# Kernel optimization log

Hardware: AMD Instinct MI355X
Metric: run time of the kernel (lower is better)

## Reference

```python
import jax, jax.numpy as jnp
import numpy as np

B, C, T, H, NCLS = 512, 22, 1000, 64, 4


def setup_inputs() -> dict:
    key = jax.random.key(0)
    ks = jax.random.split(key, 8)
    s_ih = 1.0 / np.sqrt(H)
    x = jax.random.normal(ks[0], (B, C, T), dtype=jnp.float32)
    # PyTorch LSTM params: gate order [i, f, g, o], each of size H
    W_ih = jax.random.uniform(ks[1], (4 * H, C), minval=-s_ih, maxval=s_ih, dtype=jnp.float32)
    W_hh = jax.random.uniform(ks[2], (4 * H, H), minval=-s_ih, maxval=s_ih, dtype=jnp.float32)
    b_ih = jax.random.uniform(ks[3], (4 * H,), minval=-s_ih, maxval=s_ih, dtype=jnp.float32)
    b_hh = jax.random.uniform(ks[4], (4 * H,), minval=-s_ih, maxval=s_ih, dtype=jnp.float32)
    s_fc = 1.0 / np.sqrt(H * T)
    W_fc = jax.random.uniform(ks[5], (NCLS, H * T), minval=-s_fc, maxval=s_fc, dtype=jnp.float32)
    b_fc = jax.random.uniform(ks[6], (NCLS,), minval=-s_fc, maxval=s_fc, dtype=jnp.float32)
    return {"x": x, "W_ih": W_ih, "W_hh": W_hh, "b_ih": b_ih, "b_hh": b_hh,
            "W_fc": W_fc, "b_fc": b_fc}


def _lstm(xs, W_ih, W_hh, b_ih, b_hh):
    # xs: [B, T, C] -> outputs [B, T, H]
    b = xs.shape[0]
    # precompute input projections for all timesteps: [T, B, 4H]
    x_proj = jnp.einsum('btc,gc->tbg', xs, W_ih) + (b_ih + b_hh)
    h0 = jnp.zeros((b, W_hh.shape[1]), xs.dtype)
    c0 = jnp.zeros_like(h0)

    def step(carry, xp):
        h, c = carry
        gates = xp + h @ W_hh.T  # [B, 4H]
        i, f, g, o = jnp.split(gates, 4, axis=-1)
        i = jax.nn.sigmoid(i)
        f = jax.nn.sigmoid(f)
        g = jnp.tanh(g)
        o = jax.nn.sigmoid(o)
        c = f * c + i * g
        h = o * jnp.tanh(c)
        return (h, c), h

    _, hs = jax.lax.scan(step, (h0, c0), x_proj)  # hs: [T, B, H]
    return jnp.transpose(hs, (1, 0, 2))  # [B, T, H]


def reference(x, W_ih, W_hh, b_ih, b_hh, W_fc, b_fc):
    xs = jnp.transpose(x, (0, 2, 1))  # [B, T, C]  (permute(0,2,1))
    hs = _lstm(xs, W_ih, W_hh, b_ih, b_hh)  # [B, T, H]
    flat = hs.reshape(hs.shape[0], -1)  # [B, T*H], time-major per row
    logits = flat @ W_fc.T + b_fc  # [B, 4]
    return jax.nn.softmax(logits, axis=1)
```

## Files before the change

kernel.cpp:

```cpp
#include <hip/hip_runtime.h>

#define BB   512
#define CC   22
#define TT   1000
#define HH   64
#define NCLS 4
#define FCW  (TT * HH)
#define TB   100

typedef _Float16 f16;
typedef __attribute__((ext_vector_type(2))) _Float16 h2;

__device__ __forceinline__ float sigm(float x) {
    float e = __expf(-x);
    return __builtin_amdgcn_rcpf(1.0f + e);
}
__device__ __forceinline__ float tanh_(float x) {
    float e = __expf(-2.0f * fabsf(x));
    float r = (1.0f - e) * __builtin_amdgcn_rcpf(1.0f + e);
    return copysignf(r, x);
}
__device__ __forceinline__ h2 u2h(unsigned u) {
    union { unsigned u; h2 h; } c; c.u = u; return c.h;
}
__device__ __forceinline__ unsigned h2u(h2 h) {
    union { unsigned u; h2 h; } c; c.h = h; return c.u;
}

__global__ __launch_bounds__(256) void xproj(
    const float* __restrict__ x,
    const float* __restrict__ W_ih,
    const float* __restrict__ b_ih,
    const float* __restrict__ b_hh,
    f16* __restrict__ xp)
{
    __shared__ __align__(16) float xt[CC][TB];

    const int tid = threadIdx.x;
    const int t0  = blockIdx.x * TB;
    const int b   = blockIdx.y;
    const int hid = tid >> 2;
    const int g   = tid & 3;
    const int row = g * HH + hid;

    for (int s = tid; s < CC * TB; s += 256) {
        const int c = s / TB, t = s - c * TB;
        xt[c][t] = x[((size_t)b * CC + c) * TT + t0 + t];
    }
    float wr[CC];
    #pragma unroll
    for (int c = 0; c < CC; ++c) wr[c] = W_ih[row * CC + c];
    const float bias = b_ih[row] + b_hh[row];
    __syncthreads();

    f16* op = xp + ((size_t)b * TT + t0) * 256 + tid;
    for (int t = 0; t < TB; t += 4) {
        float a0 = bias, a1 = bias, a2 = bias, a3 = bias;
        #pragma unroll
        for (int c = 0; c < CC; ++c) {
            const float4 xv = *(const float4*)&xt[c][t];
            a0 += wr[c] * xv.x; a1 += wr[c] * xv.y;
            a2 += wr[c] * xv.z; a3 += wr[c] * xv.w;
        }
        op[0]   = (f16)a0;
        op[256] = (f16)a1;
        op[512] = (f16)a2;
        op[768] = (f16)a3;
        op += 1024;
    }
}

__global__ __attribute__((amdgpu_waves_per_eu(1, 1)))
__launch_bounds__(64) void lstm_rec(
    const uint2* __restrict__ xp,
    const float* __restrict__ W_hh,
    const float* __restrict__ W_fc,
    const float* __restrict__ b_fc,
    float* __restrict__ out)
{
    __shared__ __align__(16) f16 hbuf[HH];

    const int lane = threadIdx.x;
    const int r    = blockIdx.x;

    unsigned whh[4][32];
    #pragma unroll
    for (int g = 0; g < 4; ++g) {
        const float* wr = W_hh + (g * HH + lane) * HH;
        #pragma unroll
        for (int k = 0; k < 32; ++k)
            whh[g][k] = h2u(h2{(f16)wr[2 * k], (f16)wr[2 * k + 1]});
    }
    #pragma unroll
    for (int g = 0; g < 4; ++g)
        #pragma unroll
        for (int k = 0; k < 32; ++k) asm volatile("" : "+v"(whh[g][k]));

    hbuf[lane] = (f16)0.0f;
    float c = 0.0f;
    float fc0 = 0.f, fc1 = 0.f, fc2 = 0.f, fc3 = 0.f;
    const uint2* px = xp + (size_t)r * TT * HH + lane;
    const float* p0 = W_fc + 0 * FCW + lane;
    const float* p1 = W_fc + 1 * FCW + lane;
    const float* p2 = W_fc + 2 * FCW + lane;
    const float* p3 = W_fc + 3 * FCW + lane;

    for (int t = 0; t < TT; ++t) {
        const uint2 xv = px[(size_t)t * HH];
        const float w0 = *p0, w1 = *p1, w2 = *p2, w3 = *p3;
        p0 += HH; p1 += HH; p2 += HH; p3 += HH;

        union { uint4 q[8]; h2 h[32]; } H;
        const uint4* hr = (const uint4*)hbuf;
        #pragma unroll
        for (int i = 0; i < 8; ++i) H.q[i] = hr[i];

        float a0 = 0.f, a1 = 0.f, a2 = 0.f, a3 = 0.f;
        #pragma unroll
        for (int k = 0; k < 32; ++k) {
            a0 = __builtin_amdgcn_fdot2(H.h[k], u2h(whh[0][k]), a0, false);
            a1 = __builtin_amdgcn_fdot2(H.h[k], u2h(whh[1][k]), a1, false);
            a2 = __builtin_amdgcn_fdot2(H.h[k], u2h(whh[2][k]), a2, false);
            a3 = __builtin_amdgcn_fdot2(H.h[k], u2h(whh[3][k]), a3, false);
        }
        const h2 pif = u2h(xv.x), pgo = u2h(xv.y);
        a0 += (float)pif[0]; a1 += (float)pif[1];
        a2 += (float)pgo[0]; a3 += (float)pgo[1];

        const float iv = sigm(a0), fv = sigm(a1);
        const float gv = tanh_(a2), ov = sigm(a3);
        c = fv * c + iv * gv;
        const float h = ov * tanh_(c);

        fc0 += h * w0; fc1 += h * w1; fc2 += h * w2; fc3 += h * w3;

        hbuf[lane] = (f16)h;
    }

    #pragma unroll
    for (int off = 32; off; off >>= 1) {
        fc0 += __shfl_down(fc0, off);
        fc1 += __shfl_down(fc1, off);
        fc2 += __shfl_down(fc2, off);
        fc3 += __shfl_down(fc3, off);
    }
    if (lane == 0) {
        const float l0 = fc0 + b_fc[0], l1 = fc1 + b_fc[1];
        const float l2 = fc2 + b_fc[2], l3 = fc3 + b_fc[3];
        const float m  = fmaxf(fmaxf(l0, l1), fmaxf(l2, l3));
        const float e0 = __expf(l0 - m), e1 = __expf(l1 - m);
        const float e2 = __expf(l2 - m), e3 = __expf(l3 - m);
        const float is = __builtin_amdgcn_rcpf(e0 + e1 + e2 + e3);
        float4 o; o.x = e0 * is; o.y = e1 * is; o.z = e2 * is; o.w = e3 * is;
        *(float4*)(out + r * NCLS) = o;
    }
}

#define TC   250
#define NCHUNK (TT / TC)
#define XROW 12

__global__ __attribute__((amdgpu_waves_per_eu(1, 1)))
__launch_bounds__(64) void lstm_fb(
    const float* __restrict__ x, const float* __restrict__ W_ih,
    const float* __restrict__ W_hh, const float* __restrict__ b_ih,
    const float* __restrict__ b_hh, const float* __restrict__ W_fc,
    const float* __restrict__ b_fc, float* __restrict__ out)
{
    __shared__ __align__(16) h2  xs[TC][XROW];
    __shared__ __align__(16) f16 hbuf[HH];

    const int lane = threadIdx.x;
    const int r    = blockIdx.x;

    unsigned whh[4][32];
    unsigned wih[4][11];
    float bias[4];
    #pragma unroll
    for (int g = 0; g < 4; ++g) {
        const int row = g * HH + lane;
        const float* wr = W_hh + row * HH;
        #pragma unroll
        for (int k = 0; k < 32; ++k)
            whh[g][k] = h2u(h2{(f16)wr[2 * k], (f16)wr[2 * k + 1]});
        const float* wi = W_ih + row * CC;
        #pragma unroll
        for (int k = 0; k < 11; ++k)
            wih[g][k] = h2u(h2{(f16)wi[2 * k], (f16)wi[2 * k + 1]});
        bias[g] = b_ih[row] + b_hh[row];
    }
    #pragma unroll
    for (int g = 0; g < 4; ++g) {
        #pragma unroll
        for (int k = 0; k < 32; ++k) asm volatile("" : "+v"(whh[g][k]));
        #pragma unroll
        for (int k = 0; k < 11; ++k) asm volatile("" : "+v"(wih[g][k]));
        asm volatile("" : "+v"(bias[g]));
    }

    hbuf[lane] = (f16)0.0f;
    float c = 0.0f;
    float fc0 = 0.f, fc1 = 0.f, fc2 = 0.f, fc3 = 0.f;
    const float* p0 = W_fc + 0 * FCW + lane;
    const float* p1 = W_fc + 1 * FCW + lane;
    const float* p2 = W_fc + 2 * FCW + lane;
    const float* p3 = W_fc + 3 * FCW + lane;
    const float* xrow = x + (size_t)r * (CC * TT);

    for (int chunk = 0; chunk < NCHUNK; ++chunk) {
        for (int tb = 0; tb < TC; tb += 64) {
            const int t = tb + lane;
            if (t < TC) {
                const float* gx = xrow + chunk * TC + t;
                union { h2 h[XROW]; uint4 q[3]; } U;
                #pragma unroll
                for (int k = 0; k < 11; ++k)
                    U.h[k] = h2{(f16)gx[(2 * k) * TT], (f16)gx[(2 * k + 1) * TT]};
                U.h[11] = h2{(f16)0.0f, (f16)0.0f};
                uint4* dst = (uint4*)&xs[t][0];
                dst[0] = U.q[0]; dst[1] = U.q[1]; dst[2] = U.q[2];
            }
        }
        for (int tt = 0; tt < TC; ++tt) {
            union { uint4 q[8]; h2 h[32]; } H;
            const uint4* hr = (const uint4*)hbuf;
            #pragma unroll
            for (int i = 0; i < 8; ++i) H.q[i] = hr[i];
            union { uint4 q[3]; h2 h[XROW]; } X;
            const uint4* xr = (const uint4*)&xs[tt][0];
            X.q[0] = xr[0]; X.q[1] = xr[1]; X.q[2] = xr[2];
            float w0 = *p0, w1 = *p1, w2 = *p2, w3 = *p3;
            p0 += HH; p1 += HH; p2 += HH; p3 += HH;
            float a0 = bias[0], a1 = bias[1], a2 = bias[2], a3 = bias[3];
            #pragma unroll
            for (int k = 0; k < 11; ++k) {
                a0 = __builtin_amdgcn_fdot2(X.h[k], u2h(wih[0][k]), a0, false);
                a1 = __builtin_amdgcn_fdot2(X.h[k], u2h(wih[1][k]), a1, false);
                a2 = __builtin_amdgcn_fdot2(X.h[k], u2h(wih[2][k]), a2, false);
                a3 = __builtin_amdgcn_fdot2(X.h[k], u2h(wih[3][k]), a3, false);
            }
            #pragma unroll
            for (int k = 0; k < 32; ++k) {
                a0 = __builtin_amdgcn_fdot2(H.h[k], u2h(whh[0][k]), a0, false);
                a1 = __builtin_amdgcn_fdot2(H.h[k], u2h(whh[1][k]), a1, false);
                a2 = __builtin_amdgcn_fdot2(H.h[k], u2h(whh[2][k]), a2, false);
                a3 = __builtin_amdgcn_fdot2(H.h[k], u2h(whh[3][k]), a3, false);
            }
            const float iv = sigm(a0), fv = sigm(a1);
            const float gv = tanh_(a2), ov = sigm(a3);
            c = fv * c + iv * gv;
            const float h = ov * tanh_(c);
            fc0 += h * w0; fc1 += h * w1; fc2 += h * w2; fc3 += h * w3;
            hbuf[lane] = (f16)h;
        }
    }
    #pragma unroll
    for (int off = 32; off; off >>= 1) {
        fc0 += __shfl_down(fc0, off);
        fc1 += __shfl_down(fc1, off);
        fc2 += __shfl_down(fc2, off);
        fc3 += __shfl_down(fc3, off);
    }
    if (lane == 0) {
        const float l0 = fc0 + b_fc[0], l1 = fc1 + b_fc[1];
        const float l2 = fc2 + b_fc[2], l3 = fc3 + b_fc[3];
        const float m  = fmaxf(fmaxf(l0, l1), fmaxf(l2, l3));
        const float e0 = __expf(l0 - m), e1 = __expf(l1 - m);
        const float e2 = __expf(l2 - m), e3 = __expf(l3 - m);
        const float is = __builtin_amdgcn_rcpf(e0 + e1 + e2 + e3);
        float4 o; o.x = e0 * is; o.y = e1 * is; o.z = e2 * is; o.w = e3 * is;
        *(float4*)(out + r * NCLS) = o;
    }
}

extern "C" void kernel_launch(void* const* d_in, const int* in_sizes, int n_in,
                              void* d_out, int out_size, void* d_ws, size_t ws_size,
                              hipStream_t stream) {
    const float* x    = (const float*)d_in[0];
    const float* W_ih = (const float*)d_in[1];
    const float* W_hh = (const float*)d_in[2];
    const float* b_ih = (const float*)d_in[3];
    const float* b_hh = (const float*)d_in[4];
    const float* W_fc = (const float*)d_in[5];
    const float* b_fc = (const float*)d_in[6];
    float* out = (float*)d_out;

    const size_t need = (size_t)BB * TT * HH * 4 * sizeof(f16);
    if (d_ws != nullptr && ws_size >= need) {
        f16* xp = (f16*)d_ws;
        xproj<<<dim3(TT / TB, BB), 256, 0, stream>>>(x, W_ih, b_ih, b_hh, xp);
        lstm_rec<<<BB, 64, 0, stream>>>((const uint2*)xp, W_hh, W_fc, b_fc, out);
    } else {
        lstm_fb<<<BB, 64, 0, stream>>>(x, W_ih, W_hh, b_ih, b_hh, W_fc, b_fc, out);
    }
}
```

Before: 729.5 us.

## Prefetch projections two steps ahead, unroll recurrence by two, pack xproj stores

The recurrent loop is unrolled by two, and the input projections and FC weights for steps t+2 and t+3 are loaded ahead of time, so global memory latency is hidden behind the serial dot-product chain. The projection bias is now the initial value of the fdot2 accumulators instead of being added afterwards. The xproj kernel has each thread compute two gate rows and write them as one packed half2 word, halving the number of store instructions. The cost is higher register pressure in a kernel that already holds W_hh in registers, which could cause spills.

```diff
diff --git a/kernel.cpp b/kernel.cpp
--- a/kernel.cpp
+++ b/kernel.cpp
@@ -26,47 +26,61 @@
 __device__ __forceinline__ unsigned h2u(h2 h) {
     union { unsigned u; h2 h; } c; c.h = h; return c.u;
 }
+__device__ __forceinline__ unsigned pack2(float a, float b) {
+    union { unsigned u; h2 h; } c;
+    c.h = h2{(f16)a, (f16)b};
+    return c.u;
+}
 
 __global__ __launch_bounds__(256) void xproj(
     const float* __restrict__ x,
     const float* __restrict__ W_ih,
     const float* __restrict__ b_ih,
     const float* __restrict__ b_hh,
-    f16* __restrict__ xp)
+    unsigned* __restrict__ xp)
 {
     __shared__ __align__(16) float xt[CC][TB];
 
     const int tid = threadIdx.x;
     const int t0  = blockIdx.x * TB;
     const int b   = blockIdx.y;
-    const int hid = tid >> 2;
-    const int g   = tid & 3;
-    const int row = g * HH + hid;
+    const int th  = tid >> 7;
+    const int p   = tid & 127;
+    const int hid = p >> 1;
+    const int gp  = p & 1;
+    const int ra  = (2 * gp) * HH + hid;
+    const int rb  = (2 * gp + 1) * HH + hid;
 
     for (int s = tid; s < CC * TB; s += 256) {
         const int c = s / TB, t = s - c * TB;
         xt[c][t] = x[((size_t)b * CC + c) * TT + t0 + t];
     }
-    float wr[CC];
-    #pragma unroll
-    for (int c = 0; c < CC; ++c) wr[c] = W_ih[row * CC + c];
-    const float bias = b_ih[row] + b_hh[row];
+    float wa[CC], wb[CC];
+    #pragma unroll
+    for (int c = 0; c < CC; ++c) {
+        wa[c] = W_ih[ra * CC + c];
+        wb[c] = W_ih[rb * CC + c];
+    }
+    const float ba = b_ih[ra] + b_hh[ra];
+    const float bb = b_ih[rb] + b_hh[rb];
     __syncthreads();
 
-    f16* op = xp + ((size_t)b * TT + t0) * 256 + tid;
-    for (int t = 0; t < TB; t += 4) {
-        float a0 = bias, a1 = bias, a2 = bias, a3 = bias;
+    unsigned* op = xp + ((size_t)b * TT + t0) * 128 + p;
+    for (int tb = th * 4; tb < TB; tb += 8) {
+        float a0 = ba, a1 = ba, a2 = ba, a3 = ba;
+        float c0 = bb, c1 = bb, c2 = bb, c3 = bb;
         #pragma unroll
         for (int c = 0; c < CC; ++c) {
-            const float4 xv = *(const float4*)&xt[c][t];
-            a0 += wr[c] * xv.x; a1 += wr[c] * xv.y;
-            a2 += wr[c] * xv.z; a3 += wr[c] * xv.w;
-        }
-        op[0]   = (f16)a0;
-        op[256] = (f16)a1;
-        op[512] = (f16)a2;
-        op[768] = (f16)a3;
-        op += 1024;
+            const float4 xv = *(const float4*)&xt[c][tb];
+            a0 += wa[c] * xv.x; a1 += wa[c] * xv.y;
+            a2 += wa[c] * xv.z; a3 += wa[c] * xv.w;
+            c0 += wb[c] * xv.x; c1 += wb[c] * xv.y;
+            c2 += wb[c] * xv.z; c3 += wb[c] * xv.w;
+        }
+        op[(size_t)(tb + 0) * 128] = pack2(a0, c0);
+        op[(size_t)(tb + 1) * 128] = pack2(a1, c1);
+        op[(size_t)(tb + 2) * 128] = pack2(a2, c2);
+        op[(size_t)(tb + 3) * 128] = pack2(a3, c3);
     }
 }
 
@@ -100,41 +114,74 @@
     float c = 0.0f;
     float fc0 = 0.f, fc1 = 0.f, fc2 = 0.f, fc3 = 0.f;
     const uint2* px = xp + (size_t)r * TT * HH + lane;
-    const float* p0 = W_fc + 0 * FCW + lane;
-    const float* p1 = W_fc + 1 * FCW + lane;
-    const float* p2 = W_fc + 2 * FCW + lane;
-    const float* p3 = W_fc + 3 * FCW + lane;
-
-    for (int t = 0; t < TT; ++t) {
-        const uint2 xv = px[(size_t)t * HH];
-        const float w0 = *p0, w1 = *p1, w2 = *p2, w3 = *p3;
-        p0 += HH; p1 += HH; p2 += HH; p3 += HH;
-
-        union { uint4 q[8]; h2 h[32]; } H;
-        const uint4* hr = (const uint4*)hbuf;
-        #pragma unroll
-        for (int i = 0; i < 8; ++i) H.q[i] = hr[i];
-
-        float a0 = 0.f, a1 = 0.f, a2 = 0.f, a3 = 0.f;
-        #pragma unroll
-        for (int k = 0; k < 32; ++k) {
-            a0 = __builtin_amdgcn_fdot2(H.h[k], u2h(whh[0][k]), a0, false);
-            a1 = __builtin_amdgcn_fdot2(H.h[k], u2h(whh[1][k]), a1, false);
-            a2 = __builtin_amdgcn_fdot2(H.h[k], u2h(whh[2][k]), a2, false);
-            a3 = __builtin_amdgcn_fdot2(H.h[k], u2h(whh[3][k]), a3, false);
-        }
-        const h2 pif = u2h(xv.x), pgo = u2h(xv.y);
-        a0 += (float)pif[0]; a1 += (float)pif[1];
-        a2 += (float)pgo[0]; a3 += (float)pgo[1];
-
-        const float iv = sigm(a0), fv = sigm(a1);
-        const float gv = tanh_(a2), ov = sigm(a3);
-        c = fv * c + iv * gv;
-        const float h = ov * tanh_(c);
-
-        fc0 += h * w0; fc1 += h * w1; fc2 += h * w2; fc3 += h * w3;
-
-        hbuf[lane] = (f16)h;
+    const float* pf0 = W_fc + 0 * FCW + lane;
+    const float* pf1 = W_fc + 1 * FCW + lane;
+    const float* pf2 = W_fc + 2 * FCW + lane;
+    const float* pf3 = W_fc + 3 * FCW + lane;
+
+    uint2 xvA = px[0];
+    uint2 xvB = px[HH];
+    float wA0 = pf0[0],  wA1 = pf1[0],  wA2 = pf2[0],  wA3 = pf3[0];
+    float wB0 = pf0[HH], wB1 = pf1[HH], wB2 = pf2[HH], wB3 = pf3[HH];
+
+    for (int t = 0; t < TT; t += 2) {
+        const size_t o2 = (size_t)((t + 2 < TT) ? t + 2 : TT - 1) * HH;
+        const size_t o3 = (size_t)((t + 3 < TT) ? t + 3 : TT - 1) * HH;
+        const uint2 xv2 = px[o2];
+        const uint2 xv3 = px[o3];
+        const float w20 = pf0[o2], w21 = pf1[o2], w22 = pf2[o2], w23 = pf3[o2];
+        const float w30 = pf0[o3], w31 = pf1[o3], w32 = pf2[o3], w33 = pf3[o3];
+
+        {
+            union { uint4 q[8]; h2 h[32]; } H;
+            const uint4* hr = (const uint4*)hbuf;
+            #pragma unroll
+            for (int i = 0; i < 8; ++i) H.q[i] = hr[i];
+
+            const h2 pif = u2h(xvA.x), pgo = u2h(xvA.y);
+            float a0 = (float)pif[0], a1 = (float)pif[1];
+            float a2 = (float)pgo[0], a3 = (float)pgo[1];
+            #pragma unroll
+            for (int k = 0; k < 32; ++k) {
+                a0 = __builtin_amdgcn_fdot2(H.h[k], u2h(whh[0][k]), a0, false);
+                a1 = __builtin_amdgcn_fdot2(H.h[k], u2h(whh[1][k]), a1, false);
+                a2 = __builtin_amdgcn_fdot2(H.h[k], u2h(whh[2][k]), a2, false);
+                a3 = __builtin_amdgcn_fdot2(H.h[k], u2h(whh[3][k]), a3, false);
+            }
+            const float iv = sigm(a0), fv = sigm(a1);
+            const float gv = tanh_(a2), ov = sigm(a3);
+            c = fv * c + iv * gv;
+            const float h = ov * tanh_(c);
+            fc0 += h * wA0; fc1 += h * wA1; fc2 += h * wA2; fc3 += h * wA3;
+            hbuf[lane] = (f16)h;
+        }
+        {
+            union { uint4 q[8]; h2 h[32]; } H;
+            const uint4* hr = (const uint4*)hbuf;
+            #pragma unroll
+            for (int i = 0; i < 8; ++i) H.q[i] = hr[i];
+
+            const h2 pif = u2h(xvB.x), pgo = u2h(xvB.y);
+            float a0 = (float)pif[0], a1 = (float)pif[1];
+            float a2 = (float)pgo[0], a3 = (float)pgo[1];
+            #pragma unroll
+            for (int k = 0; k < 32; ++k) {
+                a0 = __builtin_amdgcn_fdot2(H.h[k], u2h(whh[0][k]), a0, false);
+                a1 = __builtin_amdgcn_fdot2(H.h[k], u2h(whh[1][k]), a1, false);
+                a2 = __builtin_amdgcn_fdot2(H.h[k], u2h(whh[2][k]), a2, false);
+                a3 = __builtin_amdgcn_fdot2(H.h[k], u2h(whh[3][k]), a3, false);
+            }
+            const float iv = sigm(a0), fv = sigm(a1);
+            const float gv = tanh_(a2), ov = sigm(a3);
+            c = fv * c + iv * gv;
+            const float h = ov * tanh_(c);
+            fc0 += h * wB0; fc1 += h * wB1; fc2 += h * wB2; fc3 += h * wB3;
+            hbuf[lane] = (f16)h;
+        }
+
+        xvA = xv2; xvB = xv3;
+        wA0 = w20; wA1 = w21; wA2 = w22; wA3 = w23;
+        wB0 = w30; wB1 = w31; wB2 = w32; wB3 = w33;
     }
 
     #pragma unroll
@@ -287,7 +334,7 @@
 
     const size_t need = (size_t)BB * TT * HH * 4 * sizeof(f16);
     if (d_ws != nullptr && ws_size >= need) {
-        f16* xp = (f16*)d_ws;
+        unsigned* xp = (unsigned*)d_ws;
         xproj<<<dim3(TT / TB, BB), 256, 0, stream>>>(x, W_ih, b_ih, b_hh, xp);
         lstm_rec<<<BB, 64, 0, stream>>>((const uint2*)xp, W_hh, W_fc, b_fc, out);
     } else {
```

Result: slower. 756.1 us (+3.6%).

## Defer FC reduction out of the recurrence, prefetch xproj, use fdot2 input projection

Applied to the files above, without the earlier changes.

The recurrent kernel no longer loads four W_fc values per step inside the serial time loop. It stores h for 250-step chunks in LDS and runs the FC dot product after each chunk. It also prefetches the input projection three steps ahead with a rotating register queue, and folds the projection into the accumulator init. The xproj kernel is reorganised to convert x and W_ih to fp16 pairs and use fdot2, writing packed uint2 per hidden unit, which adds fp16 rounding of the inputs and weights.

```diff
diff --git a/kernel.cpp b/kernel.cpp
--- a/kernel.cpp
+++ b/kernel.cpp
@@ -6,7 +6,8 @@
 #define HH   64
 #define NCLS 4
 #define FCW  (TT * HH)
-#define TB   100
+#define TBX  200
+#define TCF  250
 
 typedef _Float16 f16;
 typedef __attribute__((ext_vector_type(2))) _Float16 h2;
@@ -25,6 +26,11 @@
 }
 __device__ __forceinline__ unsigned h2u(h2 h) {
     union { unsigned u; h2 h; } c; c.h = h; return c.u;
+}
+__device__ __forceinline__ unsigned pack2(float a, float b) {
+    union { unsigned u; h2 h; } c;
+    c.h = h2{(f16)a, (f16)b};
+    return c.u;
 }
 
 __global__ __launch_bounds__(256) void xproj(
@@ -32,41 +38,53 @@
     const float* __restrict__ W_ih,
     const float* __restrict__ b_ih,
     const float* __restrict__ b_hh,
-    f16* __restrict__ xp)
+    uint2* __restrict__ xp)
 {
-    __shared__ __align__(16) float xt[CC][TB];
+    __shared__ __align__(16) h2 xt[TBX][12];
 
     const int tid = threadIdx.x;
-    const int t0  = blockIdx.x * TB;
+    const int t0  = blockIdx.x * TBX;
     const int b   = blockIdx.y;
-    const int hid = tid >> 2;
-    const int g   = tid & 3;
-    const int row = g * HH + hid;
-
-    for (int s = tid; s < CC * TB; s += 256) {
-        const int c = s / TB, t = s - c * TB;
-        xt[c][t] = x[((size_t)b * CC + c) * TT + t0 + t];
-    }
-    float wr[CC];
-    #pragma unroll
-    for (int c = 0; c < CC; ++c) wr[c] = W_ih[row * CC + c];
-    const float bias = b_ih[row] + b_hh[row];
+    const int hid = tid & 63;
+    const int tsub = tid >> 6;
+
+    if (tid < TBX) {
+        const float* gx = x + (size_t)b * (CC * TT) + t0 + tid;
+        union { h2 h[12]; uint4 q[3]; } U;
+        #pragma unroll
+        for (int k = 0; k < 11; ++k)
+            U.h[k] = h2{(f16)gx[(2 * k) * TT], (f16)gx[(2 * k + 1) * TT]};
+        U.h[11] = h2{(f16)0.0f, (f16)0.0f};
+        uint4* dst = (uint4*)&xt[tid][0];
+        dst[0] = U.q[0]; dst[1] = U.q[1]; dst[2] = U.q[2];
+    }
+
+    unsigned wih[4][11];
+    float bias[4];
+    #pragma unroll
+    for (int g = 0; g < 4; ++g) {
+        const float* wi = W_ih + (g * HH + hid) * CC;
+        #pragma unroll
+        for (int k = 0; k < 11; ++k)
+            wih[g][k] = h2u(h2{(f16)wi[2 * k], (f16)wi[2 * k + 1]});
+        bias[g] = b_ih[g * HH + hid] + b_hh[g * HH + hid];
+    }
     __syncthreads();
 
-    f16* op = xp + ((size_t)b * TT + t0) * 256 + tid;
-    for (int t = 0; t < TB; t += 4) {
-        float a0 = bias, a1 = bias, a2 = bias, a3 = bias;
-        #pragma unroll
-        for (int c = 0; c < CC; ++c) {
-            const float4 xv = *(const float4*)&xt[c][t];
-            a0 += wr[c] * xv.x; a1 += wr[c] * xv.y;
-            a2 += wr[c] * xv.z; a3 += wr[c] * xv.w;
-        }
-        op[0]   = (f16)a0;
-        op[256] = (f16)a1;
-        op[512] = (f16)a2;
-        op[768] = (f16)a3;
-        op += 1024;
+    uint2* op = xp + ((size_t)b * TT + t0) * 64 + hid;
+    for (int t = tsub; t < TBX; t += 4) {
+        union { uint4 q[3]; h2 h[12]; } X;
+        const uint4* xr = (const uint4*)&xt[t][0];
+        X.q[0] = xr[0]; X.q[1] = xr[1]; X.q[2] = xr[2];
+        float a0 = bias[0], a1 = bias[1], a2 = bias[2], a3 = bias[3];
+        #pragma unroll
+        for (int k = 0; k < 11; ++k) {
+            a0 = __builtin_amdgcn_fdot2(X.h[k], u2h(wih[0][k]), a0, false);
+            a1 = __builtin_amdgcn_fdot2(X.h[k], u2h(wih[1][k]), a1, false);
+            a2 = __builtin_amdgcn_fdot2(X.h[k], u2h(wih[2][k]), a2, false);
+            a3 = __builtin_amdgcn_fdot2(X.h[k], u2h(wih[3][k]), a3, false);
+        }
+        op[(size_t)t * 64] = uint2{pack2(a0, a1), pack2(a2, a3)};
     }
 }
 
@@ -78,7 +96,7 @@
     const float* __restrict__ b_fc,
     float* __restrict__ out)
 {
-    __shared__ __align__(16) f16 hbuf[HH];
+    __shared__ __align__(16) f16 hst[TCF][HH];
 
     const int lane = threadIdx.x;
     const int r    = blockIdx.x;
@@ -96,45 +114,62 @@
         #pragma unroll
         for (int k = 0; k < 32; ++k) asm volatile("" : "+v"(whh[g][k]));
 
-    hbuf[lane] = (f16)0.0f;
+    hst[TCF - 1][lane] = (f16)0.0f;
     float c = 0.0f;
     float fc0 = 0.f, fc1 = 0.f, fc2 = 0.f, fc3 = 0.f;
     const uint2* px = xp + (size_t)r * TT * HH + lane;
-    const float* p0 = W_fc + 0 * FCW + lane;
-    const float* p1 = W_fc + 1 * FCW + lane;
-    const float* p2 = W_fc + 2 * FCW + lane;
-    const float* p3 = W_fc + 3 * FCW + lane;
-
-    for (int t = 0; t < TT; ++t) {
-        const uint2 xv = px[(size_t)t * HH];
-        const float w0 = *p0, w1 = *p1, w2 = *p2, w3 = *p3;
-        p0 += HH; p1 += HH; p2 += HH; p3 += HH;
-
-        union { uint4 q[8]; h2 h[32]; } H;
-        const uint4* hr = (const uint4*)hbuf;
-        #pragma unroll
-        for (int i = 0; i < 8; ++i) H.q[i] = hr[i];
-
-        float a0 = 0.f, a1 = 0.f, a2 = 0.f, a3 = 0.f;
-        #pragma unroll
-        for (int k = 0; k < 32; ++k) {
-            a0 = __builtin_amdgcn_fdot2(H.h[k], u2h(whh[0][k]), a0, false);
-            a1 = __builtin_amdgcn_fdot2(H.h[k], u2h(whh[1][k]), a1, false);
-            a2 = __builtin_amdgcn_fdot2(H.h[k], u2h(whh[2][k]), a2, false);
-            a3 = __builtin_amdgcn_fdot2(H.h[k], u2h(whh[3][k]), a3, false);
-        }
-        const h2 pif = u2h(xv.x), pgo = u2h(xv.y);
-        a0 += (float)pif[0]; a1 += (float)pif[1];
-        a2 += (float)pgo[0]; a3 += (float)pgo[1];
-
-        const float iv = sigm(a0), fv = sigm(a1);
-        const float gv = tanh_(a2), ov = sigm(a3);
-        c = fv * c + iv * gv;
-        const float h = ov * tanh_(c);
-
-        fc0 += h * w0; fc1 += h * w1; fc2 += h * w2; fc3 += h * w3;
-
-        hbuf[lane] = (f16)h;
+
+    uint2 xvA = px[0];
+    uint2 xvB = px[HH];
+    uint2 xvC = px[2 * HH];
+
+    for (int chunk = 0; chunk < 4; ++chunk) {
+        const int T0 = chunk * TCF;
+
+        for (int tt = 0; tt < TCF; ++tt) {
+            const int t = T0 + tt;
+
+            const int tp = (t + 3 < TT) ? t + 3 : TT - 1;
+            const uint2 xvN = px[(size_t)tp * HH];
+
+            const int pr = (tt == 0) ? TCF - 1 : tt - 1;
+            union { uint4 q[8]; h2 h[32]; } H;
+            const uint4* hr = (const uint4*)&hst[pr][0];
+            #pragma unroll
+            for (int i = 0; i < 8; ++i) H.q[i] = hr[i];
+
+            const h2 pif = u2h(xvA.x), pgo = u2h(xvA.y);
+            float a0 = (float)pif[0], a1 = (float)pif[1];
+            float a2 = (float)pgo[0], a3 = (float)pgo[1];
+            #pragma unroll
+            for (int k = 0; k < 32; ++k) {
+                a0 = __builtin_amdgcn_fdot2(H.h[k], u2h(whh[0][k]), a0, false);
+                a1 = __builtin_amdgcn_fdot2(H.h[k], u2h(whh[1][k]), a1, false);
+                a2 = __builtin_amdgcn_fdot2(H.h[k], u2h(whh[2][k]), a2, false);
+                a3 = __builtin_amdgcn_fdot2(H.h[k], u2h(whh[3][k]), a3, false);
+            }
+
+            const float iv = sigm(a0), fv = sigm(a1);
+            const float gv = tanh_(a2), ov = sigm(a3);
+            c = fv * c + iv * gv;
+            const float h = ov * tanh_(c);
+
+            hst[tt][lane] = (f16)h;
+
+            xvA = xvB; xvB = xvC; xvC = xvN;
+        }
+
+        const float* w0 = W_fc + 0 * FCW + (size_t)T0 * HH + lane;
+        const float* w1 = W_fc + 1 * FCW + (size_t)T0 * HH + lane;
+        const float* w2 = W_fc + 2 * FCW + (size_t)T0 * HH + lane;
+        const float* w3 = W_fc + 3 * FCW + (size_t)T0 * HH + lane;
+        for (int tt = 0; tt < TCF; ++tt) {
+            const float hv = (float)hst[tt][lane];
+            fc0 += hv * w0[(size_t)tt * HH];
+            fc1 += hv * w1[(size_t)tt * HH];
+            fc2 += hv * w2[(size_t)tt * HH];
+            fc3 += hv * w3[(size_t)tt * HH];
+        }
     }
 
     #pragma unroll
@@ -287,9 +322,9 @@
 
     const size_t need = (size_t)BB * TT * HH * 4 * sizeof(f16);
     if (d_ws != nullptr && ws_size >= need) {
-        f16* xp = (f16*)d_ws;
-        xproj<<<dim3(TT / TB, BB), 256, 0, stream>>>(x, W_ih, b_ih, b_hh, xp);
-        lstm_rec<<<BB, 64, 0, stream>>>((const uint2*)xp, W_hh, W_fc, b_fc, out);
+        uint2* xp = (uint2*)d_ws;
+        xproj<<<dim3(TT / TBX, BB), 256, 0, stream>>>(x, W_ih, b_ih, b_hh, xp);
+        lstm_rec<<<BB, 64, 0, stream>>>(xp, W_hh, W_fc, b_fc, out);
     } else {
         lstm_fb<<<BB, 64, 0, stream>>>(x, W_ih, W_hh, b_ih, b_hh, W_fc, b_fc, out);
     }
```

New measurement: 655.4 us. 10.2% less time.
